# Kernel tuning notes

Measured on AMD Instinct MI355X. Metric: run time of the kernel, lower is better.

## Reference

```python
import jax, jax.numpy as jnp
import numpy as np

C = 96        # d_model
DI = 192      # d_inner = 2*C
N = 16        # d_state
R = 6         # dt_rank = ceil(C/16)
K = 4         # scan directions
B_, H_, W_ = 2, 48, 48


def setup_inputs():
    key = jax.random.key(0)
    ks = jax.random.split(key, 12)
    def rn(k, shape, s=0.02):
        return jax.random.normal(k, shape, jnp.float32) * s
    # S4D-real A init and realistic dt bias (inverse softplus of dt in [1e-3, 1e-1])
    A = jnp.tile(jnp.arange(1, N + 1, dtype=jnp.float32), (K, DI, 1))
    dt = jax.random.uniform(ks[0], (K, DI), jnp.float32, 1e-3, 1e-1)
    inv_softplus_dt = dt + jnp.log(-jnp.expm1(-dt))
    return {
        "x": jax.random.normal(ks[1], (B_, C, H_, W_), jnp.float32),
        "ln1_w": jnp.ones((C,), jnp.float32), "ln1_b": jnp.zeros((C,), jnp.float32),
        "in_proj_w": rn(ks[2], (2 * DI, C)),
        "conv_w": rn(ks[3], (DI, 1, 3, 3), 0.1), "conv_b": jnp.zeros((DI,), jnp.float32),
        "x_proj_w": rn(ks[4], (K, R + 2 * N, DI)),
        "dt_proj_w": rn(ks[5], (K, DI, R), 0.1), "dt_proj_b": inv_softplus_dt,
        "A_log": jnp.log(A), "Ds": jnp.ones((K, DI), jnp.float32),
        "out_norm_w": jnp.ones((DI,), jnp.float32), "out_norm_b": jnp.zeros((DI,), jnp.float32),
        "out_proj_w": rn(ks[6], (C, DI)),
        "ln2_w": jnp.ones((C,), jnp.float32), "ln2_b": jnp.zeros((C,), jnp.float32),
        "fc1_w": rn(ks[7], (C, C)), "fc1_b": jnp.zeros((C,), jnp.float32),
        "fc2_w": rn(ks[8], (C, C)), "fc2_b": jnp.zeros((C,), jnp.float32),
        "proj_w": rn(ks[9], (1, C)), "proj_b": jnp.zeros((1,), jnp.float32),
    }


def _layernorm(x, w, b, eps=1e-5):
    mu = x.mean(-1, keepdims=True)
    var = x.var(-1, keepdims=True)
    return (x - mu) * jax.lax.rsqrt(var + eps) * w + b


def _selective_scan(u, delta, A, Bm, Cm, D):
    # u, delta: (B,K,D,L); A: (K,D,N); Bm, Cm: (B,K,N,L); D: (K,D)
    dA = jnp.exp(jnp.einsum('bkdl,kdn->lbkdn', delta, A))
    dBu = jnp.einsum('bkdl,bknl->lbkdn', delta * u, Bm)
    Ct = jnp.moveaxis(Cm, -1, 0)  # (L,B,K,N)
    h0 = jnp.zeros(dA.shape[1:], u.dtype)
    def step(h, inp):
        dA_t, dBu_t, C_t = inp
        h = dA_t * h + dBu_t
        y = jnp.einsum('bkdn,bkn->bkd', h, C_t)
        return h, y
    _, ys = jax.lax.scan(step, h0, (dA, dBu, Ct))
    y = jnp.moveaxis(ys, 0, -1)  # (B,K,D,L)
    return y + u * D[None, :, :, None]


def _ss2d(x, in_proj_w, conv_w, conv_b, x_proj_w, dt_proj_w, dt_proj_b,
          A_log, Ds, out_norm_w, out_norm_b, out_proj_w):
    Bsz, H, W, _ = x.shape
    L = H * W
    xz = x @ in_proj_w.T                      # (B,H,W,2*DI)
    xh, z = jnp.split(xz, 2, axis=-1)
    xc = xh.transpose(0, 3, 1, 2)             # (B,DI,H,W)
    xc = jax.lax.conv_general_dilated(
        xc, conv_w, (1, 1), ((1, 1), (1, 1)),
        feature_group_count=DI,
        dimension_numbers=('NCHW', 'OIHW', 'NCHW')) + conv_b[None, :, None, None]
    xc = jax.nn.silu(xc)
    # cross-scan: 4 directions (row-major, col-major, and their reverses)
    xf = xc.reshape(Bsz, DI, L)
    xt = xc.transpose(0, 1, 3, 2).reshape(Bsz, DI, L)
    xs2 = jnp.stack([xf, xt], axis=1)
    xs = jnp.concatenate([xs2, jnp.flip(xs2, axis=-1)], axis=1)   # (B,4,DI,L)
    x_dbl = jnp.einsum('bkdl,kcd->bkcl', xs, x_proj_w)
    dts, Bm, Cm = jnp.split(x_dbl, [R, R + N], axis=2)
    delta = jnp.einsum('bkrl,kdr->bkdl', dts, dt_proj_w) + dt_proj_b[None, :, :, None]
    delta = jax.nn.softplus(delta)
    A = -jnp.exp(A_log)
    out_y = _selective_scan(xs, delta, A, Bm, Cm, Ds)             # (B,4,DI,L)
    # cross-merge: undo flips/transposes and sum
    inv_y = jnp.flip(out_y[:, 2:4], axis=-1)
    wh_y = out_y[:, 1].reshape(Bsz, DI, W, H).transpose(0, 1, 3, 2).reshape(Bsz, DI, L)
    invwh_y = inv_y[:, 1].reshape(Bsz, DI, W, H).transpose(0, 1, 3, 2).reshape(Bsz, DI, L)
    y = out_y[:, 0] + inv_y[:, 0] + wh_y + invwh_y                # (B,DI,L)
    y = _layernorm(y.transpose(0, 2, 1), out_norm_w, out_norm_b).reshape(Bsz, H, W, DI)
    y = y * jax.nn.silu(z)
    return y @ out_proj_w.T


def reference(x, ln1_w, ln1_b, in_proj_w, conv_w, conv_b, x_proj_w, dt_proj_w,
              dt_proj_b, A_log, Ds, out_norm_w, out_norm_b, out_proj_w,
              ln2_w, ln2_b, fc1_w, fc1_b, fc2_w, fc2_b, proj_w, proj_b):
    xh = x.transpose(0, 2, 3, 1)   # (B,H,W,C)
    # VSSBlock (pre-norm): x = x + SS2D(LN(x)); x = x + MLP(LN(x))
    h1 = _layernorm(xh, ln1_w, ln1_b)
    xh = xh + _ss2d(h1, in_proj_w, conv_w, conv_b, x_proj_w, dt_proj_w,
                    dt_proj_b, A_log, Ds, out_norm_w, out_norm_b, out_proj_w)
    h2 = _layernorm(xh, ln2_w, ln2_b)
    xh = xh + (jax.nn.gelu(h2 @ fc1_w.T + fc1_b, approximate=False) @ fc2_w.T + fc2_b)
    # 1x1 conv projector + sigmoid
    y = xh @ proj_w.T + proj_b     # (B,H,W,1)
    return jax.nn.sigmoid(y).transpose(0, 3, 1, 2)
```

## Files before the change

kernel.cpp:

```cpp
#include <hip/hip_runtime.h>
#include <cstdint>

static constexpr int LSZ = 2304;
static constexpr int CBS = 96;
static constexpr int DIN = 192;
static constexpr int NST = 16;
static constexpr int HHT = 48;
static constexpr int WWD = 48;
static constexpr int CHN = 16;
static constexpr int CHL = 144;

static constexpr size_t OFF_XCONV = 0;
static constexpr size_t OFF_SILUZ = 884736;
static constexpr size_t OFF_XC    = 1769472;
static constexpr size_t OFF_XCT   = 2654208;
static constexpr size_t OFF_XDBL  = 3538944;
static constexpr size_t OFF_DELTA = 4239360;
static constexpr size_t OFF_HFIN  = 7778304;
static constexpr size_t OFF_SUMD  = 8171520;
static constexpr size_t OFF_HIN   = 8196096;
static constexpr size_t OFF_Y4    = 8589312;
static constexpr size_t OFF_XH1   = 12128256;
static constexpr size_t OFF_WT    = 12570624;

__device__ __forceinline__ float f4get(const float4& v, int i) {
    return i == 0 ? v.x : i == 1 ? v.y : i == 2 ? v.z : v.w;
}

__device__ __forceinline__ float rotadd16(float v) {
    int m;
    m = __builtin_amdgcn_update_dpp(0, __float_as_int(v), 0x128, 0xf, 0xf, false); v += __int_as_float(m);
    m = __builtin_amdgcn_update_dpp(0, __float_as_int(v), 0x124, 0xf, 0xf, false); v += __int_as_float(m);
    m = __builtin_amdgcn_update_dpp(0, __float_as_int(v), 0x122, 0xf, 0xf, false); v += __int_as_float(m);
    m = __builtin_amdgcn_update_dpp(0, __float_as_int(v), 0x121, 0xf, 0xf, false); v += __int_as_float(m);
    return v;
}

__global__ __launch_bounds__(256) void kPrep(const float* __restrict__ Wp,
    const float* __restrict__ Wo, const float* __restrict__ W1,
    const float* __restrict__ W2, float* __restrict__ wt) {
    int e = blockIdx.x * 256 + threadIdx.x;
    if (e < 36864) {
        int c = e / 384, t = e % 384;
        wt[e] = Wp[t * 96 + c];
    } else if (e < 55296) {
        int e2 = e - 36864; int dd = e2 / 96, cc = e2 % 96;
        wt[e] = Wo[cc * 192 + dd];
    } else if (e < 64512) {
        int e2 = e - 55296; int jj = e2 / 96, ii = e2 % 96;
        wt[e] = W1[ii * 96 + jj];
    } else if (e < 73728) {
        int e2 = e - 64512; int jj = e2 / 96, ii = e2 % 96;
        wt[e] = W2[ii * 96 + jj];
    }
}

__global__ __launch_bounds__(384) void kA(const float* __restrict__ x,
    const float* __restrict__ ln1w, const float* __restrict__ ln1b,
    const float* __restrict__ Wt, float* __restrict__ xconv, float* __restrict__ siluz) {
    int blk = blockIdx.x; int b = blk / 144; int s0 = (blk % 144) * 16;
    int tid = threadIdx.x;
    __shared__ float xln[96][20];
    __shared__ float mu16[16], ir16[16];
#pragma unroll
    for (int it = 0; it < 4; ++it) {
        int e = it * 384 + tid; int c = e >> 4, si = e & 15;
        xln[c][si] = x[((size_t)b * CBS + c) * LSZ + s0 + si];
    }
    __syncthreads();
    if (tid < 16) {
        float s1 = 0.f, s2 = 0.f;
#pragma unroll 8
        for (int c = 0; c < 96; ++c) { float v = xln[c][tid]; s1 += v; s2 += v * v; }
        float mu = s1 * (1.f / 96.f);
        mu16[tid] = mu; ir16[tid] = rsqrtf(s2 * (1.f / 96.f) - mu * mu + 1e-5f);
    }
    __syncthreads();
#pragma unroll
    for (int it = 0; it < 4; ++it) {
        int e = it * 384 + tid; int c = e >> 4, si = e & 15;
        xln[c][si] = (xln[c][si] - mu16[si]) * ir16[si] * ln1w[c] + ln1b[c];
    }
    __syncthreads();
    float acc[16];
#pragma unroll
    for (int i = 0; i < 16; ++i) acc[i] = 0.f;
    for (int c = 0; c < 96; ++c) {
        float wv = Wt[c * 384 + tid];
#pragma unroll
        for (int i = 0; i < 16; ++i) acc[i] = fmaf(wv, xln[c][i], acc[i]);
    }
    if (tid < DIN) {
        size_t base = ((size_t)b * DIN + tid) * LSZ + s0;
#pragma unroll
        for (int q = 0; q < 4; ++q) {
            float4 v = make_float4(acc[4 * q], acc[4 * q + 1], acc[4 * q + 2], acc[4 * q + 3]);
            *(float4*)(xconv + base + 4 * q) = v;
        }
    } else {
        int t = tid - DIN;
#pragma unroll
        for (int si = 0; si < 16; ++si) {
            float z = acc[si];
            siluz[((size_t)b * LSZ + s0 + si) * DIN + t] = z / (1.f + __expf(-z));
        }
    }
}

__global__ __launch_bounds__(256) void kB(const float* __restrict__ xconv,
    const float* __restrict__ cw, const float* __restrict__ cb,
    float* __restrict__ xc, float* __restrict__ xcT) {
    int bd = blockIdx.x;
    int d = bd % DIN;
    int tid = threadIdx.x;
    __shared__ float inp[2304];
    __shared__ float outp[48 * 49];
    const float* src = xconv + (size_t)bd * LSZ;
#pragma unroll
    for (int i = 0; i < 9; ++i) inp[i * 256 + tid] = src[i * 256 + tid];
    float w0 = cw[d * 9 + 0], w1 = cw[d * 9 + 1], w2 = cw[d * 9 + 2];
    float w3 = cw[d * 9 + 3], w4 = cw[d * 9 + 4], w5 = cw[d * 9 + 5];
    float w6 = cw[d * 9 + 6], w7 = cw[d * 9 + 7], w8 = cw[d * 9 + 8];
    float bias = cb[d];
    __syncthreads();
#pragma unroll
    for (int i = 0; i < 9; ++i) {
        int s = i * 256 + tid; int h = s / 48, w = s % 48;
        float acc = bias;
        bool hn = h > 0, hp = h < 47, wn = w > 0, wp = w < 47;
        if (hn) {
            if (wn) acc = fmaf(inp[s - 49], w0, acc);
            acc = fmaf(inp[s - 48], w1, acc);
            if (wp) acc = fmaf(inp[s - 47], w2, acc);
        }
        if (wn) acc = fmaf(inp[s - 1], w3, acc);
        acc = fmaf(inp[s], w4, acc);
        if (wp) acc = fmaf(inp[s + 1], w5, acc);
        if (hp) {
            if (wn) acc = fmaf(inp[s + 47], w6, acc);
            acc = fmaf(inp[s + 48], w7, acc);
            if (wp) acc = fmaf(inp[s + 49], w8, acc);
        }
        float r = acc / (1.f + __expf(-acc));
        xc[(size_t)bd * LSZ + s] = r;
        outp[h * 49 + w] = r;
    }
    __syncthreads();
#pragma unroll
    for (int i = 0; i < 9; ++i) {
        int p = i * 256 + tid;
        int w = p / 48, h = p % 48;
        xcT[(size_t)bd * LSZ + p] = outp[h * 49 + w];
    }
}

__global__ __launch_bounds__(256) void kC1(const float* __restrict__ xc,
    const float* __restrict__ xcT, const float* __restrict__ xpw, float* __restrict__ xdbl) {
    int blk = blockIdx.x; int lt = blk % 36; int k = (blk / 36) & 3; int b = blk / 144;
    int l0 = lt * 64;
    __shared__ float xs[DIN][64];
    const float* src = ((k & 1) ? xcT : xc) + (size_t)b * DIN * LSZ;
    bool fwd = (k < 2);
    int tid = threadIdx.x;
#pragma unroll
    for (int i = 0; i < 48; ++i) {
        int e = i * 256 + tid; int d = e >> 6, ll = e & 63;
        int l = l0 + ll; int sl = fwd ? l : (LSZ - 1 - l);
        xs[d][ll] = src[(size_t)d * LSZ + sl];
    }
    __syncthreads();
    int c0 = tid >> 6, ll = tid & 63;
    float acc[10];
#pragma unroll
    for (int j = 0; j < 10; ++j) acc[j] = 0.f;
    for (int d0 = 0; d0 < DIN; d0 += 16) {
        float xv[16];
#pragma unroll
        for (int i = 0; i < 16; ++i) xv[i] = xs[d0 + i][ll];
#pragma unroll
        for (int j = 0; j < 10; ++j) {
            int c = j * 4 + c0;
            if (c < 38) {
                const float4* wr = (const float4*)(xpw + ((size_t)(k * 38 + c)) * DIN + d0);
                float4 q0 = wr[0], q1 = wr[1], q2 = wr[2], q3 = wr[3];
                acc[j] += xv[0] * q0.x + xv[1] * q0.y + xv[2] * q0.z + xv[3] * q0.w
                        + xv[4] * q1.x + xv[5] * q1.y + xv[6] * q1.z + xv[7] * q1.w
                        + xv[8] * q2.x + xv[9] * q2.y + xv[10] * q2.z + xv[11] * q2.w
                        + xv[12] * q3.x + xv[13] * q3.y + xv[14] * q3.z + xv[15] * q3.w;
            }
        }
    }
    size_t base = ((size_t)(b * 4 + k) * LSZ + l0 + ll) * 38;
#pragma unroll
    for (int j = 0; j < 10; ++j) {
        int c = j * 4 + c0;
        if (c < 38) xdbl[base + c] = acc[j];
    }
}

__global__ __launch_bounds__(256) void kC2(const float* __restrict__ xdbl,
    const float* __restrict__ dtw, const float* __restrict__ dtb, float* __restrict__ delta) {
    int blk = blockIdx.x; int lt = blk % 36; int k = (blk / 36) & 3; int b = blk / 144;
    int l0 = lt * 64;
    int tid = threadIdx.x;
    __shared__ float dts[6][64];
    __shared__ float wsh[DIN * 6];
    __shared__ float bsh[DIN];
    size_t xb = ((size_t)(b * 4 + k) * LSZ + l0) * 38;
    for (int e = tid; e < 384; e += 256) { int r = e >> 6, ll = e & 63; dts[r][ll] = xdbl[xb + (size_t)ll * 38 + r]; }
    for (int e = tid; e < 1152; e += 256) wsh[e] = dtw[k * 1152 + e];
    if (tid < DIN) bsh[tid] = dtb[k * DIN + tid];
    __syncthreads();
    int dsub = tid >> 6, ll = tid & 63;
    for (int j = 0; j < 48; ++j) {
        int d = j * 4 + dsub;
        float acc = bsh[d];
#pragma unroll
        for (int r = 0; r < 6; ++r) acc = fmaf(dts[r][ll], wsh[d * 6 + r], acc);
        float sp = (acc > 20.f) ? acc : log1pf(__expf(acc));
        delta[((size_t)(b * 4 + k) * DIN + d) * LSZ + l0 + ll] = sp;
    }
}

__global__ __launch_bounds__(256) void kD1(const float* __restrict__ delta,
    const float* __restrict__ xc, const float* __restrict__ xcT,
    const float* __restrict__ xdbl, const float* __restrict__ A_log,
    float* __restrict__ hfin, float* __restrict__ sumd) {
    int g = blockIdx.x;
    int tid = threadIdx.x;
    int n = tid & 15; int c = tid >> 4;
    int d = g % DIN; int bk = g / DIN; int k = bk & 3; int b = bk >> 2;
    float An = -__expf(A_log[((size_t)(k * DIN + d)) * NST + n]);
    const float* dp = delta + (size_t)g * LSZ;
    const float* ub = ((k & 1) ? xcT : xc) + ((size_t)(b * DIN + d)) * LSZ;
    bool fwd = (k < 2);
    int l0 = c * CHL;
    const float* bp = xdbl + ((size_t)bk * LSZ + l0) * 38 + 6 + n;
    float h = 0.f, sd = 0.f;
    for (int j0 = 0; j0 < CHL; j0 += 4) {
        float4 dv = *(const float4*)(dp + l0 + j0);
        float4 uv;
        if (fwd) uv = *(const float4*)(ub + l0 + j0);
        else { float4 tv = *(const float4*)(ub + (LSZ - 4) - l0 - j0); uv = make_float4(tv.w, tv.z, tv.y, tv.x); }
#pragma unroll
        for (int jj = 0; jj < 4; ++jj) {
            float dl = f4get(dv, jj), ul = f4get(uv, jj);
            float bn = bp[(j0 + jj) * 38];
            float da = __expf(dl * An);
            h = fmaf(da, h, dl * ul * bn);
            sd += dl;
        }
    }
    hfin[((size_t)g * CHN + c) * NST + n] = h;
    if (n == 0) sumd[g * CHN + c] = sd;
}

__global__ __launch_bounds__(256) void kDc(const float* __restrict__ hfin,
    const float* __restrict__ sumd, const float* __restrict__ A_log, float* __restrict__ hin) {
    int t = blockIdx.x * 256 + threadIdx.x;
    int n = t & 15; int g = t >> 4;
    int d = g % DIN; int k = (g / DIN) & 3;
    float An = -__expf(A_log[((size_t)(k * DIN + d)) * NST + n]);
    float h = 0.f;
#pragma unroll
    for (int c = 0; c < CHN; ++c) {
        hin[((size_t)g * CHN + c) * NST + n] = h;
        float ap = __expf(An * sumd[g * CHN + c]);
        h = fmaf(ap, h, hfin[((size_t)g * CHN + c) * NST + n]);
    }
}

__global__ __launch_bounds__(256) void kD2(const float* __restrict__ delta,
    const float* __restrict__ xc, const float* __restrict__ xcT,
    const float* __restrict__ xdbl, const float* __restrict__ A_log,
    const float* __restrict__ Dsp, const float* __restrict__ hin, float* __restrict__ yk) {
    int g = blockIdx.x;
    int tid = threadIdx.x;
    int n = tid & 15; int c = tid >> 4;
    int d = g % DIN; int bk = g / DIN; int k = bk & 3; int b = bk >> 2;
    __shared__ float ybuf[2304];
    float An = -__expf(A_log[((size_t)(k * DIN + d)) * NST + n]);
    const float* ub = ((k & 1) ? xcT : xc) + ((size_t)(b * DIN + d)) * LSZ;
    bool fwd = (k < 2);
    int l0 = c * CHL;
    const float* bp = xdbl + ((size_t)bk * LSZ + l0) * 38 + 6 + n;
    const float* cp = xdbl + ((size_t)bk * LSZ + l0) * 38 + 22 + n;
    const float* dp = delta + (size_t)g * LSZ;
    float h = hin[((size_t)g * CHN + c) * NST + n];
    float Dkd = Dsp[k * DIN + d];
    for (int j0 = 0; j0 < CHL; j0 += 4) {
        float4 dv = *(const float4*)(dp + l0 + j0);
        float4 uv;
        if (fwd) uv = *(const float4*)(ub + l0 + j0);
        else { float4 tv = *(const float4*)(ub + (LSZ - 4) - l0 - j0); uv = make_float4(tv.w, tv.z, tv.y, tv.x); }
#pragma unroll
        for (int jj = 0; jj < 4; ++jj) {
            float dl = f4get(dv, jj), ul = f4get(uv, jj);
            float bn = bp[(j0 + jj) * 38];
            float cn = cp[(j0 + jj) * 38];
            float da = __expf(dl * An);
            h = fmaf(da, h, dl * ul * bn);
            float y = rotadd16(h * cn);
            if (n == 0) ybuf[l0 + j0 + jj] = y + Dkd * ul;
        }
    }
    __syncthreads();
    float* yo = yk + (size_t)g * LSZ;
#pragma unroll
    for (int i = 0; i < 9; ++i) yo[i * 256 + tid] = ybuf[i * 256 + tid];
}

__global__ __launch_bounds__(256) void kM(const float* __restrict__ yk, float* __restrict__ ym) {
    int blk = blockIdx.x;
    int b = blk / DIN; int d = blk % DIN;
    int tid = threadIdx.x;
    __shared__ float buf[4][2304];
#pragma unroll
    for (int k = 0; k < 4; ++k) {
        const float* src = yk + ((size_t)((b * 4 + k) * DIN + d)) * LSZ;
#pragma unroll
        for (int i = 0; i < 9; ++i) buf[k][i * 256 + tid] = src[i * 256 + tid];
    }
    __syncthreads();
    float* dst = ym + ((size_t)blk) * LSZ;
#pragma unroll
    for (int i = 0; i < 9; ++i) {
        int s = i * 256 + tid; int hh = s / 48, ww = s % 48;
        int p = ww * 48 + hh;
        dst[s] = buf[0][s] + buf[2][2303 - s] + buf[1][p] + buf[3][2303 - p];
    }
}

__global__ __launch_bounds__(192) void kE(const float* __restrict__ ym,
    const float* __restrict__ siluz, const float* __restrict__ x,
    const float* __restrict__ onw, const float* __restrict__ onb,
    const float* __restrict__ WoT, float* __restrict__ xh1) {
    int blk = blockIdx.x; int b = blk / 144; int s0 = (blk % 144) * 16;
    int tid = threadIdx.x;
    __shared__ float yl[DIN][17];
    __shared__ float mu16[16], ir16[16];
#pragma unroll
    for (int it = 0; it < 16; ++it) {
        int e = it * 192 + tid; int d = e >> 4, si = e & 15;
        yl[d][si] = ym[((size_t)(b * DIN + d)) * LSZ + s0 + si];
    }
    __syncthreads();
    if (tid < 16) {
        float s1 = 0.f, s2 = 0.f;
        for (int c = 0; c < DIN; ++c) { float v = yl[c][tid]; s1 += v; s2 += v * v; }
        float mu = s1 * (1.f / 192.f);
        mu16[tid] = mu; ir16[tid] = rsqrtf(s2 * (1.f / 192.f) - mu * mu + 1e-5f);
    }
    __syncthreads();
#pragma unroll
    for (int si = 0; si < 16; ++si) {
        float v = yl[tid][si];
        v = (v - mu16[si]) * ir16[si] * onw[tid] + onb[tid];
        yl[tid][si] = v * siluz[((size_t)b * LSZ + s0 + si) * DIN + tid];
    }
    __syncthreads();
    int tp = tid % 96, half = tid / 96;
    float acc[8];
#pragma unroll
    for (int i = 0; i < 8; ++i) acc[i] = 0.f;
    for (int d2 = 0; d2 < DIN; ++d2) {
        float wv = WoT[d2 * 96 + tp];
#pragma unroll
        for (int i = 0; i < 8; ++i) acc[i] = fmaf(wv, yl[d2][half * 8 + i], acc[i]);
    }
#pragma unroll
    for (int i = 0; i < 8; ++i) {
        int si = half * 8 + i;
        xh1[((size_t)b * LSZ + s0 + si) * CBS + tp] =
            x[((size_t)b * CBS + tp) * LSZ + s0 + si] + acc[i];
    }
}

__global__ __launch_bounds__(192) void kF(const float* __restrict__ xh1,
    const float* __restrict__ l2w, const float* __restrict__ l2b,
    const float* __restrict__ W1T, const float* __restrict__ b1,
    const float* __restrict__ W2T, const float* __restrict__ b2,
    const float* __restrict__ pw, const float* __restrict__ pb, float* __restrict__ out) {
    int blk = blockIdx.x; int b = blk / 144; int s0 = (blk % 144) * 16;
    int tid = threadIdx.x;
    __shared__ float xo[96][17];
    __shared__ float aa[96][17];
    __shared__ float mu16[16], ir16[16];
#pragma unroll
    for (int it = 0; it < 8; ++it) {
        int e = it * 192 + tid; int si = e / 96, cc = e % 96;
        xo[cc][si] = xh1[((size_t)b * LSZ + s0 + si) * CBS + cc];
    }
    __syncthreads();
    if (tid < 16) {
        float s1 = 0.f, s2 = 0.f;
        for (int c = 0; c < 96; ++c) { float v = xo[c][tid]; s1 += v; s2 += v * v; }
        float mu = s1 * (1.f / 96.f);
        mu16[tid] = mu; ir16[tid] = rsqrtf(s2 * (1.f / 96.f) - mu * mu + 1e-5f);
    }
    __syncthreads();
#pragma unroll
    for (int it = 0; it < 8; ++it) {
        int e = it * 192 + tid; int si = e / 96, cc = e % 96;
        aa[cc][si] = (xo[cc][si] - mu16[si]) * ir16[si] * l2w[cc] + l2b[cc];
    }
    __syncthreads();
    int tp = tid % 96, half = tid / 96;
    float acc[8];
#pragma unroll
    for (int i = 0; i < 8; ++i) acc[i] = 0.f;
    for (int j = 0; j < 96; ++j) {
        float wv = W1T[j * 96 + tp];
#pragma unroll
        for (int i = 0; i < 8; ++i) acc[i] = fmaf(wv, aa[j][half * 8 + i], acc[i]);
    }
    __syncthreads();
#pragma unroll
    for (int i = 0; i < 8; ++i) {
        float tv = acc[i] + b1[tp];
        aa[tp][half * 8 + i] = 0.5f * tv * (1.f + erff(tv * 0.70710678118654752f));
    }
    __syncthreads();
    float acc2[8];
#pragma unroll
    for (int i = 0; i < 8; ++i) acc2[i] = 0.f;
    for (int j = 0; j < 96; ++j) {
        float wv = W2T[j * 96 + tp];
#pragma unroll
        for (int i = 0; i < 8; ++i) acc2[i] = fmaf(wv, aa[j][half * 8 + i], acc2[i]);
    }
    __syncthreads();
#pragma unroll
    for (int i = 0; i < 8; ++i) {
        float xf = xo[tp][half * 8 + i] + acc2[i] + b2[tp];
        aa[tp][half * 8 + i] = xf * pw[tp];
    }
    __syncthreads();
    if (tid < 16) {
        float ssum = 0.f;
        for (int c = 0; c < 96; ++c) ssum += aa[c][tid];
        out[(size_t)b * LSZ + s0 + tid] = 1.f / (1.f + __expf(-(ssum + pb[0])));
    }
}

extern "C" void kernel_launch(void* const* d_in, const int* in_sizes, int n_in,
                              void* d_out, int out_size, void* d_ws, size_t ws_size,
                              hipStream_t stream) {
    const float* x    = (const float*)d_in[0];
    const float* ln1w = (const float*)d_in[1];
    const float* ln1b = (const float*)d_in[2];
    const float* Wp   = (const float*)d_in[3];
    const float* cw   = (const float*)d_in[4];
    const float* cb   = (const float*)d_in[5];
    const float* xpw  = (const float*)d_in[6];
    const float* dtw  = (const float*)d_in[7];
    const float* dtb  = (const float*)d_in[8];
    const float* Alog = (const float*)d_in[9];
    const float* Dsp  = (const float*)d_in[10];
    const float* onw  = (const float*)d_in[11];
    const float* onb  = (const float*)d_in[12];
    const float* Wo   = (const float*)d_in[13];
    const float* l2w  = (const float*)d_in[14];
    const float* l2b  = (const float*)d_in[15];
    const float* W1   = (const float*)d_in[16];
    const float* b1   = (const float*)d_in[17];
    const float* W2   = (const float*)d_in[18];
    const float* b2   = (const float*)d_in[19];
    const float* pw   = (const float*)d_in[20];
    const float* pb   = (const float*)d_in[21];

    float* ws    = (float*)d_ws;
    float* xconv = ws + OFF_XCONV;
    float* ym    = ws + OFF_XCONV;
    float* siluz = ws + OFF_SILUZ;
    float* xc    = ws + OFF_XC;
    float* xcT   = ws + OFF_XCT;
    float* xdbl  = ws + OFF_XDBL;
    float* delta = ws + OFF_DELTA;
    float* hfin  = ws + OFF_HFIN;
    float* sumd  = ws + OFF_SUMD;
    float* hin   = ws + OFF_HIN;
    float* yk    = ws + OFF_Y4;
    float* xh1   = ws + OFF_XH1;
    float* wt    = ws + OFF_WT;
    float* WoT   = wt + 36864;
    float* W1T   = wt + 55296;
    float* W2T   = wt + 64512;

    kPrep<<<288, 256, 0, stream>>>(Wp, Wo, W1, W2, wt);
    kA<<<288, 384, 0, stream>>>(x, ln1w, ln1b, wt, xconv, siluz);
    kB<<<384, 256, 0, stream>>>(xconv, cw, cb, xc, xcT);
    kC1<<<288, 256, 0, stream>>>(xc, xcT, xpw, xdbl);
    kC2<<<288, 256, 0, stream>>>(xdbl, dtw, dtb, delta);
    kD1<<<1536, 256, 0, stream>>>(delta, xc, xcT, xdbl, Alog, hfin, sumd);
    kDc<<<96, 256, 0, stream>>>(hfin, sumd, Alog, hin);
    kD2<<<1536, 256, 0, stream>>>(delta, xc, xcT, xdbl, Alog, Dsp, hin, yk);
    kM<<<384, 256, 0, stream>>>(yk, ym);
    kE<<<288, 192, 0, stream>>>(ym, siluz, x, onw, onb, WoT, xh1);
    kF<<<288, 192, 0, stream>>>(xh1, l2w, l2b, W1T, b1, W2T, b2, pw, pb, (float*)d_out);
}
```

Before: 217.0 us.

## Fuse chunked scan passes into one kernel with planar B/C layout

Merges the three scan kernels (chunk pass, carry combine, output pass) into a single kernel that keeps chunk final states in shared memory and does the carry combine in-block. The x_proj output is split into planar dt/B/C arrays so the scan can read B and C with float4 loads instead of stride-38 gathers. The D*u skip term moves to the merge kernel as a summed coefficient, and the exp becomes exp2 with a prescaled A. Output is stored directly per lane without the shared staging buffer. In exchange, each block runs both scan passes back to back, which raises per-block work and register use.

```diff
diff --git a/kernel.cpp b/kernel.cpp
--- a/kernel.cpp
+++ b/kernel.cpp
@@ -14,25 +14,28 @@
 static constexpr size_t OFF_SILUZ = 884736;
 static constexpr size_t OFF_XC    = 1769472;
 static constexpr size_t OFF_XCT   = 2654208;
-static constexpr size_t OFF_XDBL  = 3538944;
-static constexpr size_t OFF_DELTA = 4239360;
-static constexpr size_t OFF_HFIN  = 7778304;
-static constexpr size_t OFF_SUMD  = 8171520;
-static constexpr size_t OFF_HIN   = 8196096;
-static constexpr size_t OFF_Y4    = 8589312;
-static constexpr size_t OFF_XH1   = 12128256;
-static constexpr size_t OFF_WT    = 12570624;
+static constexpr size_t OFF_DTR   = 3538944;
+static constexpr size_t OFF_BT    = 3686400;
+static constexpr size_t OFF_CT    = 3981312;
+static constexpr size_t OFF_DELTA = 4276224;
+static constexpr size_t OFF_YK    = 7815168;
+static constexpr size_t OFF_XH1   = 11354112;
+static constexpr size_t OFF_WT    = 11796480;
 
 __device__ __forceinline__ float f4get(const float4& v, int i) {
     return i == 0 ? v.x : i == 1 ? v.y : i == 2 ? v.z : v.w;
 }
 
-__device__ __forceinline__ float rotadd16(float v) {
-    int m;
-    m = __builtin_amdgcn_update_dpp(0, __float_as_int(v), 0x128, 0xf, 0xf, false); v += __int_as_float(m);
-    m = __builtin_amdgcn_update_dpp(0, __float_as_int(v), 0x124, 0xf, 0xf, false); v += __int_as_float(m);
-    m = __builtin_amdgcn_update_dpp(0, __float_as_int(v), 0x122, 0xf, 0xf, false); v += __int_as_float(m);
-    m = __builtin_amdgcn_update_dpp(0, __float_as_int(v), 0x121, 0xf, 0xf, false); v += __int_as_float(m);
+__device__ __forceinline__ float dpp_rotadd16(float v) {
+    float t;
+    asm volatile("v_add_f32_dpp %0, %1, %1 row_ror:8 row_mask:0xf bank_mask:0xf bound_ctrl:0"
+                 : "=v"(t) : "v"(v));
+    asm volatile("v_add_f32_dpp %0, %1, %1 row_ror:4 row_mask:0xf bank_mask:0xf bound_ctrl:0"
+                 : "=v"(v) : "v"(t));
+    asm volatile("v_add_f32_dpp %0, %1, %1 row_ror:2 row_mask:0xf bank_mask:0xf bound_ctrl:0"
+                 : "=v"(t) : "v"(v));
+    asm volatile("v_add_f32_dpp %0, %1, %1 row_ror:1 row_mask:0xf bank_mask:0xf bound_ctrl:0"
+                 : "=v"(v) : "v"(t));
     return v;
 }
 
@@ -155,9 +158,11 @@
 }
 
 __global__ __launch_bounds__(256) void kC1(const float* __restrict__ xc,
-    const float* __restrict__ xcT, const float* __restrict__ xpw, float* __restrict__ xdbl) {
+    const float* __restrict__ xcT, const float* __restrict__ xpw,
+    float* __restrict__ dtr, float* __restrict__ Bt, float* __restrict__ Ct) {
     int blk = blockIdx.x; int lt = blk % 36; int k = (blk / 36) & 3; int b = blk / 144;
     int l0 = lt * 64;
+    int bk = b * 4 + k;
     __shared__ float xs[DIN][64];
     const float* src = ((k & 1) ? xcT : xc) + (size_t)b * DIN * LSZ;
     bool fwd = (k < 2);
@@ -190,131 +195,132 @@
             }
         }
     }
-    size_t base = ((size_t)(b * 4 + k) * LSZ + l0 + ll) * 38;
 #pragma unroll
     for (int j = 0; j < 10; ++j) {
         int c = j * 4 + c0;
-        if (c < 38) xdbl[base + c] = acc[j];
-    }
-}
-
-__global__ __launch_bounds__(256) void kC2(const float* __restrict__ xdbl,
+        if (c < 6) {
+            dtr[(size_t)bk * 8 * LSZ + (size_t)c * LSZ + l0 + ll] = acc[j];
+        } else if (c < 22) {
+            Bt[(size_t)bk * 16 * LSZ + (size_t)(c - 6) * LSZ + l0 + ll] = acc[j];
+        } else if (c < 38) {
+            Ct[(size_t)bk * 16 * LSZ + (size_t)(c - 22) * LSZ + l0 + ll] = acc[j];
+        }
+    }
+}
+
+__global__ __launch_bounds__(256) void kC2(const float* __restrict__ dtr,
     const float* __restrict__ dtw, const float* __restrict__ dtb, float* __restrict__ delta) {
     int blk = blockIdx.x; int lt = blk % 36; int k = (blk / 36) & 3; int b = blk / 144;
     int l0 = lt * 64;
-    int tid = threadIdx.x;
-    __shared__ float dts[6][64];
+    int bk = b * 4 + k;
+    int tid = threadIdx.x;
     __shared__ float wsh[DIN * 6];
     __shared__ float bsh[DIN];
-    size_t xb = ((size_t)(b * 4 + k) * LSZ + l0) * 38;
-    for (int e = tid; e < 384; e += 256) { int r = e >> 6, ll = e & 63; dts[r][ll] = xdbl[xb + (size_t)ll * 38 + r]; }
     for (int e = tid; e < 1152; e += 256) wsh[e] = dtw[k * 1152 + e];
     if (tid < DIN) bsh[tid] = dtb[k * DIN + tid];
-    __syncthreads();
     int dsub = tid >> 6, ll = tid & 63;
+    float dr[6];
+#pragma unroll
+    for (int r = 0; r < 6; ++r) dr[r] = dtr[(size_t)bk * 8 * LSZ + (size_t)r * LSZ + l0 + ll];
+    __syncthreads();
     for (int j = 0; j < 48; ++j) {
         int d = j * 4 + dsub;
         float acc = bsh[d];
 #pragma unroll
-        for (int r = 0; r < 6; ++r) acc = fmaf(dts[r][ll], wsh[d * 6 + r], acc);
+        for (int r = 0; r < 6; ++r) acc = fmaf(dr[r], wsh[d * 6 + r], acc);
         float sp = (acc > 20.f) ? acc : log1pf(__expf(acc));
-        delta[((size_t)(b * 4 + k) * DIN + d) * LSZ + l0 + ll] = sp;
-    }
-}
-
-__global__ __launch_bounds__(256) void kD1(const float* __restrict__ delta,
+        delta[((size_t)(bk) * DIN + d) * LSZ + l0 + ll] = sp;
+    }
+}
+
+__global__ __launch_bounds__(256) void kD(const float* __restrict__ delta,
     const float* __restrict__ xc, const float* __restrict__ xcT,
-    const float* __restrict__ xdbl, const float* __restrict__ A_log,
-    float* __restrict__ hfin, float* __restrict__ sumd) {
+    const float* __restrict__ Bt, const float* __restrict__ Ct,
+    const float* __restrict__ A_log, float* __restrict__ yk) {
     int g = blockIdx.x;
     int tid = threadIdx.x;
     int n = tid & 15; int c = tid >> 4;
     int d = g % DIN; int bk = g / DIN; int k = bk & 3; int b = bk >> 2;
-    float An = -__expf(A_log[((size_t)(k * DIN + d)) * NST + n]);
-    const float* dp = delta + (size_t)g * LSZ;
+    __shared__ float hfinL[256];
+    __shared__ float sumdL[16];
+    __shared__ float hinL[256];
+
+    float An2 = -__expf(A_log[((size_t)(k * DIN + d)) * NST + n]) * 1.44269504f;
     const float* ub = ((k & 1) ? xcT : xc) + ((size_t)(b * DIN + d)) * LSZ;
     bool fwd = (k < 2);
     int l0 = c * CHL;
-    const float* bp = xdbl + ((size_t)bk * LSZ + l0) * 38 + 6 + n;
+    const float* dp = delta + (size_t)g * LSZ + l0;
+    const float* up = fwd ? (ub + l0) : (ub + (LSZ - 4) - l0);
+    const float* bp = Bt + ((size_t)bk * 16 + n) * LSZ + l0;
+    const float* cp = Ct + ((size_t)bk * 16 + n) * LSZ + l0;
+
     float h = 0.f, sd = 0.f;
-    for (int j0 = 0; j0 < CHL; j0 += 4) {
-        float4 dv = *(const float4*)(dp + l0 + j0);
-        float4 uv;
-        if (fwd) uv = *(const float4*)(ub + l0 + j0);
-        else { float4 tv = *(const float4*)(ub + (LSZ - 4) - l0 - j0); uv = make_float4(tv.w, tv.z, tv.y, tv.x); }
-#pragma unroll
-        for (int jj = 0; jj < 4; ++jj) {
-            float dl = f4get(dv, jj), ul = f4get(uv, jj);
-            float bn = bp[(j0 + jj) * 38];
-            float da = __expf(dl * An);
-            h = fmaf(da, h, dl * ul * bn);
-            sd += dl;
-        }
-    }
-    hfin[((size_t)g * CHN + c) * NST + n] = h;
-    if (n == 0) sumd[g * CHN + c] = sd;
-}
-
-__global__ __launch_bounds__(256) void kDc(const float* __restrict__ hfin,
-    const float* __restrict__ sumd, const float* __restrict__ A_log, float* __restrict__ hin) {
-    int t = blockIdx.x * 256 + threadIdx.x;
-    int n = t & 15; int g = t >> 4;
-    int d = g % DIN; int k = (g / DIN) & 3;
-    float An = -__expf(A_log[((size_t)(k * DIN + d)) * NST + n]);
-    float h = 0.f;
-#pragma unroll
-    for (int c = 0; c < CHN; ++c) {
-        hin[((size_t)g * CHN + c) * NST + n] = h;
-        float ap = __expf(An * sumd[g * CHN + c]);
-        h = fmaf(ap, h, hfin[((size_t)g * CHN + c) * NST + n]);
-    }
-}
-
-__global__ __launch_bounds__(256) void kD2(const float* __restrict__ delta,
-    const float* __restrict__ xc, const float* __restrict__ xcT,
-    const float* __restrict__ xdbl, const float* __restrict__ A_log,
-    const float* __restrict__ Dsp, const float* __restrict__ hin, float* __restrict__ yk) {
-    int g = blockIdx.x;
-    int tid = threadIdx.x;
-    int n = tid & 15; int c = tid >> 4;
-    int d = g % DIN; int bk = g / DIN; int k = bk & 3; int b = bk >> 2;
-    __shared__ float ybuf[2304];
-    float An = -__expf(A_log[((size_t)(k * DIN + d)) * NST + n]);
-    const float* ub = ((k & 1) ? xcT : xc) + ((size_t)(b * DIN + d)) * LSZ;
-    bool fwd = (k < 2);
-    int l0 = c * CHL;
-    const float* bp = xdbl + ((size_t)bk * LSZ + l0) * 38 + 6 + n;
-    const float* cp = xdbl + ((size_t)bk * LSZ + l0) * 38 + 22 + n;
-    const float* dp = delta + (size_t)g * LSZ;
-    float h = hin[((size_t)g * CHN + c) * NST + n];
-    float Dkd = Dsp[k * DIN + d];
-    for (int j0 = 0; j0 < CHL; j0 += 4) {
-        float4 dv = *(const float4*)(dp + l0 + j0);
-        float4 uv;
-        if (fwd) uv = *(const float4*)(ub + l0 + j0);
-        else { float4 tv = *(const float4*)(ub + (LSZ - 4) - l0 - j0); uv = make_float4(tv.w, tv.z, tv.y, tv.x); }
-#pragma unroll
-        for (int jj = 0; jj < 4; ++jj) {
-            float dl = f4get(dv, jj), ul = f4get(uv, jj);
-            float bn = bp[(j0 + jj) * 38];
-            float cn = cp[(j0 + jj) * 38];
-            float da = __expf(dl * An);
-            h = fmaf(da, h, dl * ul * bn);
-            float y = rotadd16(h * cn);
-            if (n == 0) ybuf[l0 + j0 + jj] = y + Dkd * ul;
-        }
-    }
-    __syncthreads();
-    float* yo = yk + (size_t)g * LSZ;
-#pragma unroll
-    for (int i = 0; i < 9; ++i) yo[i * 256 + tid] = ybuf[i * 256 + tid];
-}
-
-__global__ __launch_bounds__(256) void kM(const float* __restrict__ yk, float* __restrict__ ym) {
+    for (int m = 0; m < 9; ++m) {
+#pragma unroll
+        for (int q = 0; q < 4; ++q) {
+            int t16 = m * 16 + q * 4;
+            float4 dv = *(const float4*)(dp + t16);
+            float4 bv = *(const float4*)(bp + t16);
+            float4 uv;
+            if (fwd) uv = *(const float4*)(up + t16);
+            else { float4 tv = *(const float4*)(up - t16); uv = make_float4(tv.w, tv.z, tv.y, tv.x); }
+#pragma unroll
+            for (int jj = 0; jj < 4; ++jj) {
+                float dl = f4get(dv, jj);
+                float da = __builtin_amdgcn_exp2f(dl * An2);
+                h = fmaf(da, h, dl * f4get(uv, jj) * f4get(bv, jj));
+                sd += dl;
+            }
+        }
+    }
+    hfinL[tid] = h;
+    if (n == 0) sumdL[c] = sd;
+    __syncthreads();
+
+    if (tid < 16) {
+        float hh = 0.f;
+#pragma unroll
+        for (int cc = 0; cc < 16; ++cc) {
+            hinL[cc * 16 + tid] = hh;
+            hh = fmaf(__builtin_amdgcn_exp2f(An2 * sumdL[cc]), hh, hfinL[cc * 16 + tid]);
+        }
+    }
+    __syncthreads();
+
+    h = hinL[tid];
+    float* yo = yk + (size_t)g * LSZ + l0 + n;
+    for (int m = 0; m < 9; ++m) {
+        float ykeep = 0.f;
+#pragma unroll
+        for (int q = 0; q < 4; ++q) {
+            int t16 = m * 16 + q * 4;
+            float4 dv = *(const float4*)(dp + t16);
+            float4 bv = *(const float4*)(bp + t16);
+            float4 cv = *(const float4*)(cp + t16);
+            float4 uv;
+            if (fwd) uv = *(const float4*)(up + t16);
+            else { float4 tv = *(const float4*)(up - t16); uv = make_float4(tv.w, tv.z, tv.y, tv.x); }
+#pragma unroll
+            for (int jj = 0; jj < 4; ++jj) {
+                float dl = f4get(dv, jj);
+                float da = __builtin_amdgcn_exp2f(dl * An2);
+                h = fmaf(da, h, dl * f4get(uv, jj) * f4get(bv, jj));
+                float p = dpp_rotadd16(h * f4get(cv, jj));
+                int tt = q * 4 + jj;
+                ykeep = (n == tt) ? p : ykeep;
+            }
+        }
+        yo[m * 16] = ykeep;
+    }
+}
+
+__global__ __launch_bounds__(256) void kM(const float* __restrict__ yk,
+    const float* __restrict__ xc, const float* __restrict__ Dsp, float* __restrict__ ym) {
     int blk = blockIdx.x;
     int b = blk / DIN; int d = blk % DIN;
     int tid = threadIdx.x;
     __shared__ float buf[4][2304];
+    float Dsum = Dsp[d] + Dsp[DIN + d] + Dsp[2 * DIN + d] + Dsp[3 * DIN + d];
 #pragma unroll
     for (int k = 0; k < 4; ++k) {
         const float* src = yk + ((size_t)((b * 4 + k) * DIN + d)) * LSZ;
@@ -322,12 +328,14 @@
         for (int i = 0; i < 9; ++i) buf[k][i * 256 + tid] = src[i * 256 + tid];
     }
     __syncthreads();
+    const float* xrow = xc + ((size_t)(b * DIN + d)) * LSZ;
     float* dst = ym + ((size_t)blk) * LSZ;
 #pragma unroll
     for (int i = 0; i < 9; ++i) {
         int s = i * 256 + tid; int hh = s / 48, ww = s % 48;
         int p = ww * 48 + hh;
-        dst[s] = buf[0][s] + buf[2][2303 - s] + buf[1][p] + buf[3][2303 - p];
+        dst[s] = buf[0][s] + buf[2][2303 - s] + buf[1][p] + buf[3][2303 - p]
+               + Dsum * xrow[s];
     }
 }
 
@@ -475,12 +483,11 @@
     float* siluz = ws + OFF_SILUZ;
     float* xc    = ws + OFF_XC;
     float* xcT   = ws + OFF_XCT;
-    float* xdbl  = ws + OFF_XDBL;
+    float* dtr   = ws + OFF_DTR;
+    float* Bt    = ws + OFF_BT;
+    float* Ct    = ws + OFF_CT;
     float* delta = ws + OFF_DELTA;
-    float* hfin  = ws + OFF_HFIN;
-    float* sumd  = ws + OFF_SUMD;
-    float* hin   = ws + OFF_HIN;
-    float* yk    = ws + OFF_Y4;
+    float* yk    = ws + OFF_YK;
     float* xh1   = ws + OFF_XH1;
     float* wt    = ws + OFF_WT;
     float* WoT   = wt + 36864;
@@ -490,12 +497,10 @@
     kPrep<<<288, 256, 0, stream>>>(Wp, Wo, W1, W2, wt);
     kA<<<288, 384, 0, stream>>>(x, ln1w, ln1b, wt, xconv, siluz);
     kB<<<384, 256, 0, stream>>>(xconv, cw, cb, xc, xcT);
-    kC1<<<288, 256, 0, stream>>>(xc, xcT, xpw, xdbl);
-    kC2<<<288, 256, 0, stream>>>(xdbl, dtw, dtb, delta);
-    kD1<<<1536, 256, 0, stream>>>(delta, xc, xcT, xdbl, Alog, hfin, sumd);
-    kDc<<<96, 256, 0, stream>>>(hfin, sumd, Alog, hin);
-    kD2<<<1536, 256, 0, stream>>>(delta, xc, xcT, xdbl, Alog, Dsp, hin, yk);
-    kM<<<384, 256, 0, stream>>>(yk, ym);
+    kC1<<<288, 256, 0, stream>>>(xc, xcT, xpw, dtr, Bt, Ct);
+    kC2<<<288, 256, 0, stream>>>(dtr, dtw, dtb, delta);
+    kD<<<1536, 256, 0, stream>>>(delta, xc, xcT, Bt, Ct, Alog, yk);
+    kM<<<384, 256, 0, stream>>>(yk, xc, Dsp, ym);
     kE<<<288, 192, 0, stream>>>(ym, siluz, x, onw, onb, WoT, xh1);
     kF<<<288, 192, 0, stream>>>(xh1, l2w, l2b, W1T, b1, W2T, b2, pw, pb, (float*)d_out);
 }
```

New measurement: 332.6 us. +53.3%, slower.
